# Performance work log

Measured on AMD Instinct MI355X. Metric: run time of the kernel, lower is better.

Reference implementation:

```python
import jax, jax.numpy as jnp
import numpy as np

# Model config (matches init_kwargs)
D_MODEL = 512
D_STATE = 64
D_CONV = 4
EXPAND = 2
NHEADS = 16
HEADDIM = 64
D_INNER = EXPAND * D_MODEL          # 1024 == NHEADS * HEADDIM
D_IN_PROJ = 2 * D_INNER + 2 * D_STATE + NHEADS  # 2192
BATCH = 2
SEQLEN = 2048


def setup_inputs() -> dict:
    key = jax.random.key(0)
    ks = jax.random.split(key, 5)
    s = 0.02  # weight scale so activations stay well-conditioned
    return {
        "x": jax.random.normal(ks[0], (BATCH, SEQLEN, D_MODEL), jnp.float32),
        "W_in": jax.random.normal(ks[1], (D_IN_PROJ, D_MODEL), jnp.float32) * s,
        "conv_w": jax.random.normal(ks[2], (D_INNER, 1, D_CONV), jnp.float32) * 0.3,
        "conv_b": jnp.zeros((D_INNER,), jnp.float32),
        "A_log": jnp.zeros((NHEADS,), jnp.float32),       # torch init: log(ones)=0
        "dt_bias": jnp.ones((NHEADS,), jnp.float32),
        "W_out": jax.random.normal(ks[3], (D_MODEL, D_INNER), jnp.float32) * s,
    }


def reference(x, W_in, conv_w, conv_b, A_log, dt_bias, W_out):
    b, l, _ = x.shape
    # in_proj (no bias)
    proj = jnp.einsum('bld,ed->ble', x, W_in)  # [b, l, D_IN_PROJ]
    z, xs, B, C, dt = jnp.split(
        proj, [D_INNER, 2 * D_INNER, 2 * D_INNER + D_STATE, 2 * D_INNER + 2 * D_STATE], axis=-1)

    # depthwise causal conv1d: torch pads (d_conv-1) on both sides then truncates
    # right to seqlen, equivalent to left-padding by d_conv-1.
    xc = jax.lax.conv_general_dilated(
        xs.transpose(0, 2, 1), conv_w,
        window_strides=(1,), padding=[(D_CONV - 1, 0)],
        dimension_numbers=('NCH', 'OIH', 'NCH'),
        feature_group_count=D_INNER)
    xc = xc + conv_b[None, :, None]
    x_ssm = jax.nn.silu(xc).transpose(0, 2, 1)           # [b, l, D_INNER]
    xh = x_ssm.reshape(b, l, NHEADS, HEADDIM)            # [b, l, h, p]

    dt = jax.nn.softplus(dt + dt_bias)                   # [b, l, h]
    A = -jnp.exp(A_log)                                  # [h]
    dA = jnp.exp(dt * A)                                 # [b, l, h], in (0,1)

    # sequential selective scan over time (lax.scan), state h: [b, h, n, p]
    def step(h, inp):
        dAt, Bt, Ct, xt = inp                            # [b,h],[b,n],[b,n],[b,h,p]
        h = dAt[:, :, None, None] * h + jnp.einsum('bn,bhp->bhnp', Bt, xt)
        y = jnp.einsum('bn,bhnp->bhp', Ct, h)
        return h, y

    h0 = jnp.zeros((b, NHEADS, D_STATE, HEADDIM), x.dtype)
    _, ys = jax.lax.scan(step, h0, (dA.transpose(1, 0, 2),
                                    B.transpose(1, 0, 2),
                                    C.transpose(1, 0, 2),
                                    xh.transpose(1, 0, 2, 3)))
    y = ys.transpose(1, 0, 2, 3).reshape(b, l, D_INNER)  # [b, l, d_inner]

    y = y * jax.nn.silu(z)                               # gated output
    return jnp.einsum('ble,de->bld', y, W_out)           # out_proj (no bias)
```

## Files before the change

kernel.cpp:

```cpp
#include <hip/hip_runtime.h>
#include <cstdint>
#include <cstddef>

#define B_N     2
#define L_N     2048
#define DMODEL  512
#define DINNER  1024
#define DSTATE  64
#define NHEADS  16
#define EPROJ   2192
#define PB      2176
#define OFF_Z   0
#define OFF_XP  1024
#define OFF_B   2048
#define OFF_C   2112
#define LC      64
#define NC      32
#define MROWS   4096

typedef unsigned short u16;
typedef unsigned int   u32;
typedef __attribute__((ext_vector_type(8))) short short8;
typedef __attribute__((ext_vector_type(4))) float floatx4;

__device__ __forceinline__ float silu_f(float v) { return v / (1.f + __expf(-v)); }

__device__ __forceinline__ u16 f2bf(float f) {
    union { float f; uint32_t u; } v; v.f = f;
    uint32_t r = (v.u + 0x7FFFu + ((v.u >> 16) & 1u)) >> 16;
    return (u16)r;
}

__device__ __forceinline__ float bf2f(u16 b) {
    union { u32 u; float f; } v; v.u = (u32)b << 16; return v.f;
}

__device__ __forceinline__ u32 pack2(float lo, float hi) {
    return (u32)f2bf(lo) | ((u32)f2bf(hi) << 16);
}

__device__ __forceinline__ float lane_bcast(float v, int n) {
    union { float f; uint32_t u; } a, b;
    a.f = v;
    b.u = __builtin_amdgcn_readlane(a.u, n);
    return b.f;
}

__device__ __forceinline__ short8 frag_ld(const u32* s, int row, int k0) {
    const u32* q = s + row * 33 + (k0 >> 1);
    union { u32 u[4]; short8 v; } r;
    r.u[0] = q[0]; r.u[1] = q[1]; r.u[2] = q[2]; r.u[3] = q[3];
    return r.v;
}

__device__ __forceinline__ void gload_lds16(const u16* g, u16* s) {
    __builtin_amdgcn_global_load_lds(
        (const __attribute__((address_space(1))) void*)g,
        (__attribute__((address_space(3))) void*)s,
        16, 0, 0);
}

__global__ __launch_bounds__(256) void cast2_kern(
    const float* __restrict__ s0, u16* __restrict__ d0, int n0,
    const float* __restrict__ s1, u16* __restrict__ d1, int n1)
{
    int i = blockIdx.x * 256 + threadIdx.x;
    const float* s; u16* d;
    if (i < n0)           { s = s0; d = d0; }
    else                  { i -= n0; if (i >= n1) return; s = s1; d = d1; }
    float4 v = ((const float4*)s)[i];
    ushort4 o;
    o.x = f2bf(v.x); o.y = f2bf(v.y); o.z = f2bf(v.z); o.w = f2bf(v.w);
    ((ushort4*)d)[i] = o;
}

template<int BM, int BN, int NPB, bool GUARD, bool PSPLIT>
__global__ __launch_bounds__(256, 2) void gemm_mfma_bt(
    const u16* __restrict__ A, const u16* __restrict__ Bt,
    float* __restrict__ Cf, u16* __restrict__ Cb, float* __restrict__ Dt,
    int M, int N, int K)
{
    constexpr int MI = BM / 32;
    constexpr int NI = BN / 32;
    constexpr int KB = 32 * NPB;
    __shared__ u16 As[2][NPB][BM * 32];
    __shared__ u16 Bs[2][NPB][BN * 32];

    const int tid = threadIdx.x;
    const int w   = tid >> 6;
    const int ln  = tid & 63;
    const int wm  = w >> 1, wn = w & 1;
    const int bm  = blockIdx.y * BM;
    const int bn  = blockIdx.x * BN;

    const int srow = ln >> 2;
    const int skq  = (ln & 3) * 8;
    const int fr = ln & 15;
    const int fq = (ln >> 4) * 8;

    floatx4 acc[MI][NI];
    const floatx4 fzero = {0.f, 0.f, 0.f, 0.f};
    #pragma unroll
    for (int mi = 0; mi < MI; ++mi)
        #pragma unroll
        for (int ni = 0; ni < NI; ++ni) acc[mi][ni] = fzero;

    auto stage = [&](int buf, int k0) {
        #pragma unroll
        for (int p = 0; p < NPB; ++p) {
            const int kp = k0 + p * 32;
            #pragma unroll
            for (int g = 0; g < BM / 16; ++g) {
                if ((g & 3) != w) continue;
                gload_lds16(A + (size_t)(bm + g * 16 + srow) * K + kp + skq,
                            &As[buf][p][g * 16 * 32]);
            }
            #pragma unroll
            for (int g = 0; g < BN / 16; ++g) {
                if ((g & 3) != w) continue;
                int rn = bn + g * 16 + srow;
                if (GUARD) rn = (rn < N) ? rn : (N - 1);
                gload_lds16(Bt + (size_t)rn * K + kp + skq,
                            &Bs[buf][p][g * 16 * 32]);
            }
        }
    };

    auto compute = [&](int buf) {
        #pragma unroll
        for (int p = 0; p < NPB; ++p) {
            short8 af[MI], bfv[NI];
            #pragma unroll
            for (int mi = 0; mi < MI; ++mi)
                af[mi] = *(const short8*)&As[buf][p][(wm * (BM / 2) + mi * 16 + fr) * 32 + fq];
            #pragma unroll
            for (int ni = 0; ni < NI; ++ni)
                bfv[ni] = *(const short8*)&Bs[buf][p][(wn * (BN / 2) + ni * 16 + fr) * 32 + fq];
            #pragma unroll
            for (int mi = 0; mi < MI; ++mi)
                #pragma unroll
                for (int ni = 0; ni < NI; ++ni)
                    acc[mi][ni] = __builtin_amdgcn_mfma_f32_16x16x32_bf16(
                        af[mi], bfv[ni], acc[mi][ni], 0, 0, 0);
        }
    };

    stage(0, 0);
    __syncthreads();

    int cur = 0;
    for (int k0 = 0; k0 + KB < K; k0 += KB) {
        stage(cur ^ 1, k0 + KB);
        compute(cur);
        __syncthreads();
        cur ^= 1;
    }
    compute(cur);

    const int cr = (ln >> 4) * 4;
    const int cc = ln & 15;
    #pragma unroll
    for (int mi = 0; mi < MI; ++mi) {
        const int row0 = bm + wm * (BM / 2) + mi * 16 + cr;
        #pragma unroll
        for (int ni = 0; ni < NI; ++ni) {
            const int col = bn + wn * (BN / 2) + ni * 16 + cc;
            #pragma unroll
            for (int r = 0; r < 4; ++r) {
                const int row = row0 + r;
                const float v = acc[mi][ni][r];
                if (PSPLIT) {
                    if (col < PB)
                        Cb[(size_t)row * PB + col] = f2bf(v);
                    else if (col < EPROJ)
                        Dt[(size_t)(col - PB) * MROWS + row] = v;
                } else {
                    Cf[(size_t)row * N + col] = v;
                }
            }
        }
    }
}

__global__ __launch_bounds__(256) void ssd_phase1(
    const u16* __restrict__ projb, const float* __restrict__ dtf,
    const float* __restrict__ cw, const float* __restrict__ cb,
    const float* __restrict__ A_log, const float* __restrict__ dt_bias,
    u16* __restrict__ hb, float* __restrict__ Pc, float* __restrict__ LaBuf,
    u32* __restrict__ xT)
{
    __shared__ u32 sBD[64 * 33];
    __shared__ u32 sXt[64 * 33];

    const int bid = blockIdx.x;
    const int c = bid & (NC - 1);
    const int h = (bid >> 5) & (NHEADS - 1);
    const int b = bid >> 9;
    const int tid = threadIdx.x;
    const int w = tid >> 6, ln = tid & 63;
    const int a = ln & 15, q = ln >> 4;
    const size_t r0 = (size_t)b * L_N + c * LC;

    float dt = dtf[(size_t)h * MROWS + r0 + ln] + dt_bias[h];
    float sp = (dt > 15.f) ? dt : log1pf(__expf(dt));
    float La = sp * (-__expf(A_log[h]));
    #pragma unroll
    for (int d = 1; d < 64; d <<= 1) {
        float up = __shfl_up(La, d, 64);
        if (ln >= d) La += up;
    }
    if (w == 0) LaBuf[(size_t)bid * 64 + ln] = La;
    const float La63 = lane_bcast(La, 63);

    const int ch = h * 64 + ln;
    const float4 w4 = *(const float4*)(cw + ch * 4);
    const float bias = cb[ch];
    const u16* xcol = projb + OFF_XP + ch;
    const size_t bbase = (size_t)b * L_N;

    float xr[3];
    #pragma unroll
    for (int i = 0; i < 3; ++i) {
        const int tl = c * LC + 16 * w - 3 + i;
        xr[i] = (tl >= 0) ? bf2f(xcol[(bbase + tl) * PB]) : 0.f;
    }

    #pragma unroll
    for (int j = 0; j < 8; ++j) {
        const int sp_ = w * 8 + j, s = sp_ * 2;
        const float xa = bf2f(xcol[(r0 + s) * PB]);
        const float xb = bf2f(xcol[(r0 + s + 1) * PB]);
        float a0 = bias, a1 = bias;
        a0 += xr[0] * w4.x; a0 += xr[1] * w4.y; a0 += xr[2] * w4.z; a0 += xa * w4.w;
        a1 += xr[1] * w4.x; a1 += xr[2] * w4.y; a1 += xa * w4.z;   a1 += xb * w4.w;
        xr[0] = xr[2]; xr[1] = xa; xr[2] = xb;
        const float x0 = silu_f(a0), x1 = silu_f(a1);
        const u32 xp = pack2(x0, x1);
        sXt[ln * 33 + sp_] = xp;
        xT[(size_t)bid * 2048 + sp_ * 64 + ln] = xp;
        const float w0 = __expf(La63 - lane_bcast(La, s));
        const float w1 = __expf(La63 - lane_bcast(La, s + 1));
        const float b0 = bf2f(projb[(r0 + s) * PB + OFF_B + ln]) * w0;
        const float b1 = bf2f(projb[(r0 + s + 1) * PB + OFF_B + ln]) * w1;
        sBD[ln * 33 + sp_] = pack2(b0, b1);
    }
    __syncthreads();

    short8 af[2], bf[4][2];
    #pragma unroll
    for (int ks = 0; ks < 2; ++ks)
        af[ks] = frag_ld(sBD, w * 16 + a, ks * 32 + q * 8);
    #pragma unroll
    for (int tn = 0; tn < 4; ++tn)
        #pragma unroll
        for (int ks = 0; ks < 2; ++ks)
            bf[tn][ks] = frag_ld(sXt, tn * 16 + a, ks * 32 + q * 8);

    const floatx4 fzero = {0.f, 0.f, 0.f, 0.f};
    floatx4 acc[4];
    #pragma unroll
    for (int tn = 0; tn < 4; ++tn) {
        acc[tn] = fzero;
        #pragma unroll
        for (int ks = 0; ks < 2; ++ks)
            acc[tn] = __builtin_amdgcn_mfma_f32_16x16x32_bf16(
                af[ks], bf[tn][ks], acc[tn], 0, 0, 0);
    }

    u16* hp = hb + (size_t)bid * 4096;
    #pragma unroll
    for (int tn = 0; tn < 4; ++tn)
        #pragma unroll
        for (int r = 0; r < 4; ++r)
            hp[(w * 16 + q * 4 + r) * 64 + tn * 16 + a] = f2bf(acc[tn][r]);
    if (tid == 0) Pc[bid] = __expf(La63);
}

__global__ __launch_bounds__(256) void ssd_phase2(
    u32* __restrict__ hb32, const float* __restrict__ Pc,
    const float* __restrict__ wsrc, u16* __restrict__ wdst, int nw)
{
    const int bid = blockIdx.x;
    if (bid >= 256) {
        const int i = (bid - 256) * 256 + threadIdx.x;
        if (i < nw) {
            float4 v = ((const float4*)wsrc)[i];
            ushort4 o;
            o.x = f2bf(v.x); o.y = f2bf(v.y); o.z = f2bf(v.z); o.w = f2bf(v.w);
            ((ushort4*)wdst)[i] = o;
        }
        return;
    }

    const int bh = bid >> 3;
    const int e = (bid & 7) * 256 + threadIdx.x;
    const size_t base = (size_t)(bh * NC) * 2048 + e;

    u32 v[NC];
    #pragma unroll
    for (int c = 0; c < NC; ++c)
        v[c] = hb32[base + (size_t)c * 2048];

    float c0 = 0.f, c1 = 0.f;
    #pragma unroll
    for (int c = 0; c < NC; ++c) {
        const u32 cur = v[c];
        const float lo = bf2f((u16)cur), hi = bf2f((u16)(cur >> 16));
        v[c] = pack2(c0, c1);
        const float Pv = Pc[bh * NC + c];
        c0 = fmaf(Pv, c0, lo);
        c1 = fmaf(Pv, c1, hi);
    }

    #pragma unroll
    for (int c = 0; c < NC; ++c)
        hb32[base + (size_t)c * 2048] = v[c];
}

__global__ __launch_bounds__(256) void ssd_phase3(
    const u16* __restrict__ projb, const u32* __restrict__ xT,
    const u16* __restrict__ hb, const float* __restrict__ LaBuf,
    u16* __restrict__ yz)
{
    __shared__ char lds[34048];
    u32* sBW   = (u32*)lds;
    u32* sC    = (u32*)(lds + 8448);
    u32* sXt   = (u32*)(lds + 16896);
    u32* sH    = (u32*)(lds + 25344);
    float* sLaF = (float*)(lds + 33792);
    float* sY  = (float*)(lds + 8448);

    const int bid = blockIdx.x;
    const int c = bid & (NC - 1);
    const int h = (bid >> 5) & (NHEADS - 1);
    const int b = bid >> 9;
    const int tid = threadIdx.x;
    const int w = tid >> 6, ln = tid & 63;
    const int a = ln & 15, q = ln >> 4;
    const int hw = ln >> 5, k32 = ln & 31;
    const size_t r0 = (size_t)b * L_N + c * LC;

    if (tid < 64) sLaF[tid] = LaBuf[(size_t)bid * 64 + tid];

    const u16* hs = hb + (size_t)bid * 4096;
    #pragma unroll
    for (int j = 0; j < 8; ++j) {
        const int rp = w * 8 + j;
        const int row = rp * 2 + hw;
        sBW[row * 33 + k32] = *(const u32*)(projb + (r0 + row) * PB + OFF_B + 2 * k32);
        sC [row * 33 + k32] = *(const u32*)(projb + (r0 + row) * PB + OFF_C + 2 * k32);
        sXt[ln * 33 + rp] = xT[(size_t)bid * 2048 + rp * 64 + ln];
        sH [ln * 33 + rp] = (u32)hs[(2 * rp) * 64 + ln]
                          | ((u32)hs[(2 * rp + 1) * 64 + ln] << 16);
    }
    __syncthreads();

    const floatx4 fzero = {0.f, 0.f, 0.f, 0.f};

    short8 cfr[2], bfr[4][2];
    #pragma unroll
    for (int ks = 0; ks < 2; ++ks)
        cfr[ks] = frag_ld(sC, w * 16 + a, ks * 32 + q * 8);
    #pragma unroll
    for (int tm = 0; tm < 4; ++tm)
        if (tm <= w)
            #pragma unroll
            for (int ks = 0; ks < 2; ++ks)
                bfr[tm][ks] = frag_ld(sBW, tm * 16 + a, ks * 32 + q * 8);
    floatx4 accS[4];
    #pragma unroll
    for (int tm = 0; tm < 4; ++tm) {
        if (tm > w) continue;
        accS[tm] = fzero;
        #pragma unroll
        for (int ks = 0; ks < 2; ++ks)
            accS[tm] = __builtin_amdgcn_mfma_f32_16x16x32_bf16(
                bfr[tm][ks], cfr[ks], accS[tm], 0, 0, 0);
    }
    __syncthreads();

    {
        const int i = w * 16 + a;
        const float Li = sLaF[i];
        #pragma unroll
        for (int tm = 0; tm < 4; ++tm) {
            const int d0 = i * 33 + tm * 8 + q * 2;
            if (tm > w) {
                sBW[d0] = 0; sBW[d0 + 1] = 0;
            } else {
                const float4 Ls = *(const float4*)(sLaF + tm * 16 + q * 4);
                float v[4];
                #pragma unroll
                for (int r = 0; r < 4; ++r) {
                    const int s = tm * 16 + q * 4 + r;
                    const float ww = (s <= i) ? __expf(Li - ((const float*)&Ls)[r]) : 0.f;
                    v[r] = accS[tm][r] * ww;
                }
                sBW[d0]     = pack2(v[0], v[1]);
                sBW[d0 + 1] = pack2(v[2], v[3]);
            }
        }
    }

    short8 hfr[4][2];
    #pragma unroll
    for (int tp = 0; tp < 4; ++tp)
        #pragma unroll
        for (int ks = 0; ks < 2; ++ks)
            hfr[tp][ks] = frag_ld(sH, tp * 16 + a, ks * 32 + q * 8);
    floatx4 accY[4];
    #pragma unroll
    for (int tp = 0; tp < 4; ++tp) {
        accY[tp] = fzero;
        #pragma unroll
        for (int ks = 0; ks < 2; ++ks)
            accY[tp] = __builtin_amdgcn_mfma_f32_16x16x32_bf16(
                cfr[ks], hfr[tp][ks], accY[tp], 0, 0, 0);
    }
    {
        const float4 Ls = *(const float4*)(sLaF + w * 16 + q * 4);
        float e4[4];
        #pragma unroll
        for (int r = 0; r < 4; ++r) e4[r] = __expf(((const float*)&Ls)[r]);
        #pragma unroll
        for (int tp = 0; tp < 4; ++tp)
            #pragma unroll
            for (int r = 0; r < 4; ++r) accY[tp][r] *= e4[r];
    }

    short8 wfr[2], xfr[4][2];
    #pragma unroll
    for (int ks = 0; ks < 2; ++ks)
        wfr[ks] = frag_ld(sBW, w * 16 + a, ks * 32 + q * 8);
    #pragma unroll
    for (int tp = 0; tp < 4; ++tp)
        #pragma unroll
        for (int ks = 0; ks < 2; ++ks)
            xfr[tp][ks] = frag_ld(sXt, tp * 16 + a, ks * 32 + q * 8);
    #pragma unroll
    for (int tp = 0; tp < 4; ++tp)
        #pragma unroll
        for (int ks = 0; ks < 2; ++ks)
            accY[tp] = __builtin_amdgcn_mfma_f32_16x16x32_bf16(
                wfr[ks], xfr[tp][ks], accY[tp], 0, 0, 0);
    __syncthreads();

    #pragma unroll
    for (int tp = 0; tp < 4; ++tp)
        #pragma unroll
        for (int r = 0; r < 4; ++r)
            sY[(w * 16 + q * 4 + r) * 66 + tp * 16 + a] = accY[tp][r];
    #pragma unroll
    for (int ii = 0; ii < 16; ++ii) {
        const int i = w * 16 + ii;
        const float y = sY[i * 66 + ln];
        const float z = bf2f(projb[(r0 + i) * PB + OFF_Z + h * 64 + ln]);
        yz[(r0 + i) * DINNER + h * 64 + ln] = f2bf(y * silu_f(z));
    }
}

extern "C" void kernel_launch(void* const* d_in, const int* in_sizes, int n_in,
                              void* d_out, int out_size, void* d_ws, size_t ws_size,
                              hipStream_t stream)
{
    const float* x       = (const float*)d_in[0];
    const float* W_in    = (const float*)d_in[1];
    const float* conv_w  = (const float*)d_in[2];
    const float* conv_b  = (const float*)d_in[3];
    const float* A_log   = (const float*)d_in[4];
    const float* dt_bias = (const float*)d_in[5];
    const float* W_out   = (const float*)d_in[6];
    float* out = (float*)d_out;

    u16*   projb = (u16*)d_ws;
    float* dtf   = (float*)(projb + (size_t)4096 * PB);
    u16*   hb    = (u16*)(dtf + (size_t)4096 * 16);
    float* Pc    = (float*)(hb + (size_t)1024 * 4096);
    float* LaBuf = Pc + 1024;
    u16*   xbf   = (u16*)(LaBuf + 1024 * 64);
    u16*   wibf  = xbf + (size_t)4096 * DMODEL;
    u16*   wobf  = wibf + (size_t)EPROJ * DMODEL;
    u16*   yzbf  = wobf + (size_t)DMODEL * DINNER;
    u32*   xT    = (u32*)(yzbf + (size_t)4096 * DINNER);

    const int M = B_N * L_N;
    const int n0 = M * DMODEL / 4, n1 = EPROJ * DMODEL / 4, n2 = DMODEL * DINNER / 4;

    cast2_kern<<<(n0 + n1 + 255) / 256, 256, 0, stream>>>(
        x, xbf, n0, W_in, wibf, n1);

    gemm_mfma_bt<128, 160, 2, true, true><<<dim3(14, M / 128), 256, 0, stream>>>(
        xbf, wibf, nullptr, projb, dtf, M, EPROJ, DMODEL);

    ssd_phase1<<<B_N * NHEADS * NC, 256, 0, stream>>>(
        projb, dtf, conv_w, conv_b, A_log, dt_bias, hb, Pc, LaBuf, xT);
    ssd_phase2<<<256 + (n2 + 255) / 256, 256, 0, stream>>>(
        (u32*)hb, Pc, W_out, wobf, n2);
    ssd_phase3<<<B_N * NHEADS * NC, 256, 0, stream>>>(
        projb, xT, hb, LaBuf, yzbf);

    gemm_mfma_bt<64, 64, 4, false, false><<<dim3(DMODEL / 64, M / 64), 256, 0, stream>>>(
        yzbf, wobf, out, nullptr, nullptr, M, DMODEL, DINNER);
}
```

Measured before the change: 136.1 us.

## Fuse all stages into one persistent kernel with software grid barriers

Replaces the six separate kernel launches with one persistent 512-block kernel. Its stages (cast, in-proj GEMM, phase1, phase2, phase3, out-proj GEMM) are separated by atomic-counter grid barriers, with one memset per call to reset the counter. This is meant to remove per-launch overhead and the idle gaps between kernels. In exchange, every block now uses one large shared buffer, occupancy is bounded by the largest stage, some stages leave blocks idle, and correctness depends on all 512 blocks being co-resident.

```diff
diff --git a/kernel.cpp b/kernel.cpp
--- a/kernel.cpp
+++ b/kernel.cpp
@@ -17,6 +17,7 @@
 #define LC      64
 #define NC      32
 #define MROWS   4096
+#define NBLK    512
 
 typedef unsigned short u16;
 typedef unsigned int   u32;
@@ -60,22 +61,20 @@
         16, 0, 0);
 }
 
-__global__ __launch_bounds__(256) void cast2_kern(
-    const float* __restrict__ s0, u16* __restrict__ d0, int n0,
-    const float* __restrict__ s1, u16* __restrict__ d1, int n1)
-{
-    int i = blockIdx.x * 256 + threadIdx.x;
-    const float* s; u16* d;
-    if (i < n0)           { s = s0; d = d0; }
-    else                  { i -= n0; if (i >= n1) return; s = s1; d = d1; }
-    float4 v = ((const float4*)s)[i];
-    ushort4 o;
-    o.x = f2bf(v.x); o.y = f2bf(v.y); o.z = f2bf(v.z); o.w = f2bf(v.w);
-    ((ushort4*)d)[i] = o;
+__device__ __forceinline__ void grid_bar(u32* cnt, u32 tgt) {
+    __syncthreads();
+    if (threadIdx.x == 0) {
+        __builtin_amdgcn_fence(__ATOMIC_RELEASE, "agent");
+        __hip_atomic_fetch_add(cnt, 1u, __ATOMIC_RELAXED, __HIP_MEMORY_SCOPE_AGENT);
+        while (__hip_atomic_load(cnt, __ATOMIC_RELAXED, __HIP_MEMORY_SCOPE_AGENT) < tgt)
+            __builtin_amdgcn_s_sleep(2);
+        __builtin_amdgcn_fence(__ATOMIC_ACQUIRE, "agent");
+    }
+    __syncthreads();
 }
 
 template<int BM, int BN, int NPB, bool GUARD, bool PSPLIT>
-__global__ __launch_bounds__(256, 2) void gemm_mfma_bt(
+__device__ __forceinline__ void gemm_body(char* smemc, int bx, int by,
     const u16* __restrict__ A, const u16* __restrict__ Bt,
     float* __restrict__ Cf, u16* __restrict__ Cb, float* __restrict__ Dt,
     int M, int N, int K)
@@ -83,15 +82,15 @@
     constexpr int MI = BM / 32;
     constexpr int NI = BN / 32;
     constexpr int KB = 32 * NPB;
-    __shared__ u16 As[2][NPB][BM * 32];
-    __shared__ u16 Bs[2][NPB][BN * 32];
+    u16* AsBase = (u16*)smemc;
+    u16* BsBase = (u16*)(smemc + (size_t)2 * NPB * BM * 32 * 2);
 
     const int tid = threadIdx.x;
     const int w   = tid >> 6;
     const int ln  = tid & 63;
     const int wm  = w >> 1, wn = w & 1;
-    const int bm  = blockIdx.y * BM;
-    const int bn  = blockIdx.x * BN;
+    const int bm  = by * BM;
+    const int bn  = bx * BN;
 
     const int srow = ln >> 2;
     const int skq  = (ln & 3) * 8;
@@ -105,6 +104,13 @@
         #pragma unroll
         for (int ni = 0; ni < NI; ++ni) acc[mi][ni] = fzero;
 
+    auto As = [&](int buf, int p) -> u16* {
+        return AsBase + ((size_t)buf * NPB + p) * (BM * 32);
+    };
+    auto Bs = [&](int buf, int p) -> u16* {
+        return BsBase + ((size_t)buf * NPB + p) * (BN * 32);
+    };
+
     auto stage = [&](int buf, int k0) {
         #pragma unroll
         for (int p = 0; p < NPB; ++p) {
@@ -113,7 +119,7 @@
             for (int g = 0; g < BM / 16; ++g) {
                 if ((g & 3) != w) continue;
                 gload_lds16(A + (size_t)(bm + g * 16 + srow) * K + kp + skq,
-                            &As[buf][p][g * 16 * 32]);
+                            As(buf, p) + g * 16 * 32);
             }
             #pragma unroll
             for (int g = 0; g < BN / 16; ++g) {
@@ -121,7 +127,7 @@
                 int rn = bn + g * 16 + srow;
                 if (GUARD) rn = (rn < N) ? rn : (N - 1);
                 gload_lds16(Bt + (size_t)rn * K + kp + skq,
-                            &Bs[buf][p][g * 16 * 32]);
+                            Bs(buf, p) + g * 16 * 32);
             }
         }
     };
@@ -132,10 +138,10 @@
             short8 af[MI], bfv[NI];
             #pragma unroll
             for (int mi = 0; mi < MI; ++mi)
-                af[mi] = *(const short8*)&As[buf][p][(wm * (BM / 2) + mi * 16 + fr) * 32 + fq];
+                af[mi] = *(const short8*)&As(buf, p)[(wm * (BM / 2) + mi * 16 + fr) * 32 + fq];
             #pragma unroll
             for (int ni = 0; ni < NI; ++ni)
-                bfv[ni] = *(const short8*)&Bs[buf][p][(wn * (BN / 2) + ni * 16 + fr) * 32 + fq];
+                bfv[ni] = *(const short8*)&Bs(buf, p)[(wn * (BN / 2) + ni * 16 + fr) * 32 + fq];
             #pragma unroll
             for (int mi = 0; mi < MI; ++mi)
                 #pragma unroll
@@ -182,17 +188,16 @@
     }
 }
 
-__global__ __launch_bounds__(256) void ssd_phase1(
+__device__ void p1_body(char* smemc, int bid,
     const u16* __restrict__ projb, const float* __restrict__ dtf,
     const float* __restrict__ cw, const float* __restrict__ cb,
     const float* __restrict__ A_log, const float* __restrict__ dt_bias,
     u16* __restrict__ hb, float* __restrict__ Pc, float* __restrict__ LaBuf,
     u32* __restrict__ xT)
 {
-    __shared__ u32 sBD[64 * 33];
-    __shared__ u32 sXt[64 * 33];
-
-    const int bid = blockIdx.x;
+    u32* sBD = (u32*)smemc;
+    u32* sXt = (u32*)(smemc + 8448);
+
     const int c = bid & (NC - 1);
     const int h = (bid >> 5) & (NHEADS - 1);
     const int b = bid >> 9;
@@ -274,26 +279,14 @@
         for (int r = 0; r < 4; ++r)
             hp[(w * 16 + q * 4 + r) * 64 + tn * 16 + a] = f2bf(acc[tn][r]);
     if (tid == 0) Pc[bid] = __expf(La63);
-}
-
-__global__ __launch_bounds__(256) void ssd_phase2(
-    u32* __restrict__ hb32, const float* __restrict__ Pc,
-    const float* __restrict__ wsrc, u16* __restrict__ wdst, int nw)
+    __syncthreads();
+}
+
+__device__ void p2_body(int bid, int tid,
+    u32* __restrict__ hb32, const float* __restrict__ Pc)
 {
-    const int bid = blockIdx.x;
-    if (bid >= 256) {
-        const int i = (bid - 256) * 256 + threadIdx.x;
-        if (i < nw) {
-            float4 v = ((const float4*)wsrc)[i];
-            ushort4 o;
-            o.x = f2bf(v.x); o.y = f2bf(v.y); o.z = f2bf(v.z); o.w = f2bf(v.w);
-            ((ushort4*)wdst)[i] = o;
-        }
-        return;
-    }
-
     const int bh = bid >> 3;
-    const int e = (bid & 7) * 256 + threadIdx.x;
+    const int e = (bid & 7) * 256 + tid;
     const size_t base = (size_t)(bh * NC) * 2048 + e;
 
     u32 v[NC];
@@ -317,12 +310,11 @@
         hb32[base + (size_t)c * 2048] = v[c];
 }
 
-__global__ __launch_bounds__(256) void ssd_phase3(
+__device__ void p3_body(char* lds, int bid,
     const u16* __restrict__ projb, const u32* __restrict__ xT,
     const u16* __restrict__ hb, const float* __restrict__ LaBuf,
     u16* __restrict__ yz)
 {
-    __shared__ char lds[34048];
     u32* sBW   = (u32*)lds;
     u32* sC    = (u32*)(lds + 8448);
     u32* sXt   = (u32*)(lds + 16896);
@@ -330,7 +322,6 @@
     float* sLaF = (float*)(lds + 33792);
     float* sY  = (float*)(lds + 8448);
 
-    const int bid = blockIdx.x;
     const int c = bid & (NC - 1);
     const int h = (bid >> 5) & (NHEADS - 1);
     const int b = bid >> 9;
@@ -457,21 +448,72 @@
         const float z = bf2f(projb[(r0 + i) * PB + OFF_Z + h * 64 + ln]);
         yz[(r0 + i) * DINNER + h * 64 + ln] = f2bf(y * silu_f(z));
     }
+    __syncthreads();
+}
+
+struct MArgs {
+    const float *x, *W_in, *conv_w, *conv_b, *A_log, *dt_bias, *W_out;
+    float* out;
+    u16* projb; float* dtf; u16* hb; float* Pc; float* LaBuf;
+    u16 *xbf, *wibf, *wobf, *yzbf; u32* xT;
+    u32* gbar;
+};
+
+__global__ __launch_bounds__(256, 2) void mega_kern(MArgs P)
+{
+    __shared__ char smem[73728];
+    const int bid = blockIdx.x;
+    const int tid = threadIdx.x;
+
+    {
+        const int n0 = MROWS * DMODEL / 4;
+        const int n1 = EPROJ * DMODEL / 4;
+        const int n2 = DMODEL * DINNER / 4;
+        const int total = n0 + n1 + n2;
+        for (int i = bid * 256 + tid; i < total; i += NBLK * 256) {
+            const float* s; u16* d; int j = i;
+            if (j < n0)      { s = P.x;    d = P.xbf; }
+            else {
+                j -= n0;
+                if (j < n1)  { s = P.W_in; d = P.wibf; }
+                else         { j -= n1; s = P.W_out; d = P.wobf; }
+            }
+            float4 v = ((const float4*)s)[j];
+            ushort4 o;
+            o.x = f2bf(v.x); o.y = f2bf(v.y); o.z = f2bf(v.z); o.w = f2bf(v.w);
+            ((ushort4*)d)[j] = o;
+        }
+    }
+    grid_bar(P.gbar, NBLK * 1);
+
+    if (bid < 448)
+        gemm_body<128, 160, 2, true, true>(smem, bid % 14, bid / 14,
+            P.xbf, P.wibf, nullptr, P.projb, P.dtf, MROWS, EPROJ, DMODEL);
+    grid_bar(P.gbar, NBLK * 2);
+
+    #pragma unroll
+    for (int it = 0; it < 2; ++it)
+        p1_body(smem, bid * 2 + it, P.projb, P.dtf, P.conv_w, P.conv_b,
+                P.A_log, P.dt_bias, P.hb, P.Pc, P.LaBuf, P.xT);
+    grid_bar(P.gbar, NBLK * 3);
+
+    if (bid < 256)
+        p2_body(bid, tid, (u32*)P.hb, P.Pc);
+    grid_bar(P.gbar, NBLK * 4);
+
+    #pragma unroll
+    for (int it = 0; it < 2; ++it)
+        p3_body(smem, bid * 2 + it, P.projb, P.xT, P.hb, P.LaBuf, P.yzbf);
+    grid_bar(P.gbar, NBLK * 5);
+
+    gemm_body<64, 64, 4, false, false>(smem, bid % 8, bid / 8,
+        P.yzbf, P.wobf, P.out, nullptr, nullptr, MROWS, DMODEL, DINNER);
 }
 
 extern "C" void kernel_launch(void* const* d_in, const int* in_sizes, int n_in,
                               void* d_out, int out_size, void* d_ws, size_t ws_size,
                               hipStream_t stream)
 {
-    const float* x       = (const float*)d_in[0];
-    const float* W_in    = (const float*)d_in[1];
-    const float* conv_w  = (const float*)d_in[2];
-    const float* conv_b  = (const float*)d_in[3];
-    const float* A_log   = (const float*)d_in[4];
-    const float* dt_bias = (const float*)d_in[5];
-    const float* W_out   = (const float*)d_in[6];
-    float* out = (float*)d_out;
-
     u16*   projb = (u16*)d_ws;
     float* dtf   = (float*)(projb + (size_t)4096 * PB);
     u16*   hb    = (u16*)(dtf + (size_t)4096 * 16);
@@ -482,23 +524,22 @@
     u16*   wobf  = wibf + (size_t)EPROJ * DMODEL;
     u16*   yzbf  = wobf + (size_t)DMODEL * DINNER;
     u32*   xT    = (u32*)(yzbf + (size_t)4096 * DINNER);
-
-    const int M = B_N * L_N;
-    const int n0 = M * DMODEL / 4, n1 = EPROJ * DMODEL / 4, n2 = DMODEL * DINNER / 4;
-
-    cast2_kern<<<(n0 + n1 + 255) / 256, 256, 0, stream>>>(
-        x, xbf, n0, W_in, wibf, n1);
-
-    gemm_mfma_bt<128, 160, 2, true, true><<<dim3(14, M / 128), 256, 0, stream>>>(
-        xbf, wibf, nullptr, projb, dtf, M, EPROJ, DMODEL);
-
-    ssd_phase1<<<B_N * NHEADS * NC, 256, 0, stream>>>(
-        projb, dtf, conv_w, conv_b, A_log, dt_bias, hb, Pc, LaBuf, xT);
-    ssd_phase2<<<256 + (n2 + 255) / 256, 256, 0, stream>>>(
-        (u32*)hb, Pc, W_out, wobf, n2);
-    ssd_phase3<<<B_N * NHEADS * NC, 256, 0, stream>>>(
-        projb, xT, hb, LaBuf, yzbf);
-
-    gemm_mfma_bt<64, 64, 4, false, false><<<dim3(DMODEL / 64, M / 64), 256, 0, stream>>>(
-        yzbf, wobf, out, nullptr, nullptr, M, DMODEL, DINNER);
-}
+    u32*   gbar  = xT + (size_t)1024 * 2048;
+
+    MArgs a;
+    a.x       = (const float*)d_in[0];
+    a.W_in    = (const float*)d_in[1];
+    a.conv_w  = (const float*)d_in[2];
+    a.conv_b  = (const float*)d_in[3];
+    a.A_log   = (const float*)d_in[4];
+    a.dt_bias = (const float*)d_in[5];
+    a.W_out   = (const float*)d_in[6];
+    a.out     = (float*)d_out;
+    a.projb = projb; a.dtf = dtf; a.hb = hb; a.Pc = Pc; a.LaBuf = LaBuf;
+    a.xbf = xbf; a.wibf = wibf; a.wobf = wobf; a.yzbf = yzbf; a.xT = xT;
+    a.gbar = gbar;
+
+    hipMemsetAsync(gbar, 0, 64, stream);
+
+    mega_kern<<<dim3(NBLK), dim3(256), 0, stream>>>(a);
+}
```

Result: slower. 338.5 us (+148.7%).
